# Kernel tuning notes

Hardware: AMD Instinct MI355X
Metric: run time of the kernel (lower is better)

The kernel has to match this reference:

```python
import jax, jax.numpy as jnp
import numpy as np

MEM_DIM = 256
NUM_CHILDREN = 16
BATCH = 16384


def setup_inputs() -> dict:
    key = jax.random.key(0)
    k1, k2, k3, k4, k5, k6 = jax.random.split(key, 6)
    D = MEM_DIM
    s = 1.0 / np.sqrt(D)
    return {
        "children_memory": jax.random.normal(k1, (NUM_CHILDREN, BATCH, D), jnp.float32),
        "children_hidden": jax.random.normal(k2, (NUM_CHILDREN, BATCH, D), jnp.float32),
        "Wf": jax.random.normal(k3, (D, D), jnp.float32) * s,
        "bf": jax.random.normal(k4, (D,), jnp.float32) * s,
        "Wiou": jax.random.normal(k5, (3 * D, D), jnp.float32) * s,
        "biou": jax.random.normal(k6, (3 * D,), jnp.float32) * s,
    }


def reference(children_memory, children_hidden, Wf, bf, Wiou, biou):
    D = Wf.shape[0]
    # sum of children hidden states over the child axis -> [B, D]
    hidden_sum = jnp.sum(children_hidden, axis=0)
    # per-child forget gates: [C, B, D]
    forget_gates = jax.nn.sigmoid(jnp.einsum("cbd,ed->cbe", children_hidden, Wf) + bf)
    # i/o/u gates from summed hidden: [B, 3D]
    iou = jnp.einsum("bd,ed->be", hidden_sum, Wiou) + biou
    input_gate = jax.nn.sigmoid(iou[:, :D])
    output_gate = jax.nn.sigmoid(iou[:, D:2 * D])
    memory_gate = jnp.tanh(iou[:, 2 * D:])
    node_memory = input_gate * memory_gate + jnp.sum(forget_gates * children_memory, axis=0)
    node_hidden = output_gate * jnp.tanh(node_memory)
    return node_memory, node_hidden
```

## Files before the change

kernel.cpp:

```cpp
#include <hip/hip_runtime.h>

#define CC 16
#define BB 16384
#define DD 256
#define BT 32
#define NT 512

typedef float f32x4 __attribute__((ext_vector_type(4)));
typedef short bf16x8 __attribute__((ext_vector_type(8)));

__device__ __forceinline__ unsigned short f2bf(float f) {
    unsigned u = __builtin_bit_cast(unsigned, f);
    u += 0x7fffu + ((u >> 16) & 1u);
    return (unsigned short)(u >> 16);
}

__device__ __forceinline__ bf16x8 pack8(f32x4 a, f32x4 b) {
    bf16x8 v;
    v[0] = (short)f2bf(a[0]); v[1] = (short)f2bf(a[1]);
    v[2] = (short)f2bf(a[2]); v[3] = (short)f2bf(a[3]);
    v[4] = (short)f2bf(b[0]); v[5] = (short)f2bf(b[1]);
    v[6] = (short)f2bf(b[2]); v[7] = (short)f2bf(b[3]);
    return v;
}

__device__ __forceinline__ float sigm(float x) {
    return __builtin_amdgcn_rcpf(1.0f + __expf(-x));
}
__device__ __forceinline__ float tanhf_(float x) {
    return 2.0f * __builtin_amdgcn_rcpf(1.0f + __expf(-2.0f * x)) - 1.0f;
}

__global__ __launch_bounds__(NT, 2) void treelstm(
    const float* __restrict__ cmem,
    const float* __restrict__ chid,
    const float* __restrict__ Wf,
    const float* __restrict__ bfv_g,
    const float* __restrict__ Wiou,
    const float* __restrict__ biou,
    float* __restrict__ out)
{
    __shared__ alignas(16) unsigned char Abuf[2][BT * DD * 2];

    const int tid  = threadIdx.x;
    const int lane = tid & 63;
    const int wid  = tid >> 6;
    const int l15  = lane & 15;
    const int l4   = lane >> 4;
    const int b0   = blockIdx.x * BT;
    const int wc0  = wid * 32;

    bf16x8 wfr[2][8];
#pragma unroll
    for (int n = 0; n < 2; ++n) {
        const float* wrow = Wf + (size_t)(wc0 + n * 16 + l15) * DD + l4 * 8;
#pragma unroll
        for (int k = 0; k < 8; ++k) {
            f32x4 x0 = *(const f32x4*)(wrow + k * 32);
            f32x4 x1 = *(const f32x4*)(wrow + k * 32 + 4);
            wfr[n][k] = pack8(x0, x1);
        }
    }
    float bfr[2];
#pragma unroll
    for (int n = 0; n < 2; ++n) bfr[n] = bfv_g[wc0 + n * 16 + l15];

    int sgoff[2], sloff[2];
#pragma unroll
    for (int g = 0; g < 2; ++g) {
        int gg = tid + g * NT;
        int r  = gg >> 5;
        int d0 = (gg & 31) * 8;
        sgoff[g] = (b0 + r) * DD + d0;
        sloff[g] = r * 512 + ((d0 * 2) ^ ((r & 7) << 4));
    }

    float hs[2][8];
#pragma unroll
    for (int g = 0; g < 2; ++g)
#pragma unroll
        for (int j = 0; j < 8; ++j) hs[g][j] = 0.0f;

    {
        f32x4 h0[2][2];
#pragma unroll
        for (int g = 0; g < 2; ++g) {
            const float* p = chid + sgoff[g];
            h0[g][0] = *(const f32x4*)p;
            h0[g][1] = *(const f32x4*)(p + 4);
        }
#pragma unroll
        for (int g = 0; g < 2; ++g) {
#pragma unroll
            for (int j = 0; j < 4; ++j) { hs[g][j] += h0[g][0][j]; hs[g][4 + j] += h0[g][1][j]; }
            *(bf16x8*)&Abuf[0][sloff[g]] = pack8(h0[g][0], h0[g][1]);
        }
    }
    __syncthreads();

    const int colbase = (l4 * 16) ^ ((l15 & 7) << 4);
    const int rb0 = l15 * 512;
    const int rb1 = (16 + l15) * 512;

    float nmv[2][2][4];
#pragma unroll
    for (int m = 0; m < 2; ++m)
#pragma unroll
        for (int n = 0; n < 2; ++n)
#pragma unroll
            for (int j = 0; j < 4; ++j) nmv[m][n][j] = 0.0f;

    const int cmbase = (b0 + l4 * 4) * DD + wc0 + l15;

    for (int c = 0; c < CC; ++c) {
        const float* cmc = cmem + (size_t)c * (BB * DD);
        float cmv[2][2][4];
#pragma unroll
        for (int m = 0; m < 2; ++m)
#pragma unroll
            for (int n = 0; n < 2; ++n)
#pragma unroll
                for (int j = 0; j < 4; ++j)
                    cmv[m][n][j] = cmc[cmbase + m * (16 * DD) + j * DD + n * 16];

        f32x4 hv[2][2];
        const bool more = (c + 1 < CC);
        if (more) {
            const float* hc = chid + (size_t)(c + 1) * (BB * DD);
#pragma unroll
            for (int g = 0; g < 2; ++g) {
                const float* p = hc + sgoff[g];
                hv[g][0] = *(const f32x4*)p;
                hv[g][1] = *(const f32x4*)(p + 4);
            }
        }

        f32x4 acc[2][2];
#pragma unroll
        for (int m = 0; m < 2; ++m)
#pragma unroll
            for (int n = 0; n < 2; ++n)
                acc[m][n] = (f32x4){bfr[n], bfr[n], bfr[n], bfr[n]};

        const unsigned char* bufc = &Abuf[c & 1][0];
#pragma unroll
        for (int k = 0; k < 8; ++k) {
            const int cb = colbase ^ (k << 6);
            bf16x8 a0 = *(const bf16x8*)(bufc + rb0 + cb);
            bf16x8 a1 = *(const bf16x8*)(bufc + rb1 + cb);
            acc[0][0] = __builtin_amdgcn_mfma_f32_16x16x32_bf16(a0, wfr[0][k], acc[0][0], 0, 0, 0);
            acc[0][1] = __builtin_amdgcn_mfma_f32_16x16x32_bf16(a0, wfr[1][k], acc[0][1], 0, 0, 0);
            acc[1][0] = __builtin_amdgcn_mfma_f32_16x16x32_bf16(a1, wfr[0][k], acc[1][0], 0, 0, 0);
            acc[1][1] = __builtin_amdgcn_mfma_f32_16x16x32_bf16(a1, wfr[1][k], acc[1][1], 0, 0, 0);
        }

        if (more) {
            unsigned char* bufn = &Abuf[(c & 1) ^ 1][0];
#pragma unroll
            for (int g = 0; g < 2; ++g) {
#pragma unroll
                for (int j = 0; j < 4; ++j) { hs[g][j] += hv[g][0][j]; hs[g][4 + j] += hv[g][1][j]; }
                *(bf16x8*)(bufn + sloff[g]) = pack8(hv[g][0], hv[g][1]);
            }
        }

#pragma unroll
        for (int m = 0; m < 2; ++m)
#pragma unroll
            for (int n = 0; n < 2; ++n)
#pragma unroll
                for (int j = 0; j < 4; ++j)
                    nmv[m][n][j] += sigm(acc[m][n][j]) * cmv[m][n][j];

        __syncthreads();
    }

#pragma unroll
    for (int g = 0; g < 2; ++g) {
        f32x4 a, b;
#pragma unroll
        for (int j = 0; j < 4; ++j) { a[j] = hs[g][j]; b[j] = hs[g][4 + j]; }
        *(bf16x8*)&Abuf[0][sloff[g]] = pack8(a, b);
    }
    __syncthreads();

    f32x4 gacc[3][2][2];
#pragma unroll
    for (int q = 0; q < 3; ++q) {
        bf16x8 wq[2][8];
#pragma unroll
        for (int n = 0; n < 2; ++n) {
            const float* wrow = Wiou + (size_t)(q * 256 + wc0 + n * 16 + l15) * DD + l4 * 8;
#pragma unroll
            for (int k = 0; k < 8; ++k) {
                f32x4 x0 = *(const f32x4*)(wrow + k * 32);
                f32x4 x1 = *(const f32x4*)(wrow + k * 32 + 4);
                wq[n][k] = pack8(x0, x1);
            }
        }
        float bq[2];
#pragma unroll
        for (int n = 0; n < 2; ++n) bq[n] = biou[q * 256 + wc0 + n * 16 + l15];
#pragma unroll
        for (int m = 0; m < 2; ++m)
#pragma unroll
            for (int n = 0; n < 2; ++n)
                gacc[q][m][n] = (f32x4){bq[n], bq[n], bq[n], bq[n]};

        const unsigned char* bufc = &Abuf[0][0];
#pragma unroll
        for (int k = 0; k < 8; ++k) {
            const int cb = colbase ^ (k << 6);
            bf16x8 a0 = *(const bf16x8*)(bufc + rb0 + cb);
            bf16x8 a1 = *(const bf16x8*)(bufc + rb1 + cb);
            gacc[q][0][0] = __builtin_amdgcn_mfma_f32_16x16x32_bf16(a0, wq[0][k], gacc[q][0][0], 0, 0, 0);
            gacc[q][0][1] = __builtin_amdgcn_mfma_f32_16x16x32_bf16(a0, wq[1][k], gacc[q][0][1], 0, 0, 0);
            gacc[q][1][0] = __builtin_amdgcn_mfma_f32_16x16x32_bf16(a1, wq[0][k], gacc[q][1][0], 0, 0, 0);
            gacc[q][1][1] = __builtin_amdgcn_mfma_f32_16x16x32_bf16(a1, wq[1][k], gacc[q][1][1], 0, 0, 0);
        }
    }

#pragma unroll
    for (int m = 0; m < 2; ++m)
#pragma unroll
        for (int n = 0; n < 2; ++n)
#pragma unroll
            for (int j = 0; j < 4; ++j) {
                float ig = sigm(gacc[0][m][n][j]);
                float og = sigm(gacc[1][m][n][j]);
                float ug = tanhf_(gacc[2][m][n][j]);
                float mm = nmv[m][n][j] + ig * ug;
                float hh = og * tanhf_(mm);
                int row = b0 + m * 16 + l4 * 4 + j;
                int col = wc0 + n * 16 + l15;
                out[(size_t)row * DD + col] = mm;
                out[(size_t)(BB * DD) + (size_t)row * DD + col] = hh;
            }
}

extern "C" void kernel_launch(void* const* d_in, const int* in_sizes, int n_in,
                              void* d_out, int out_size, void* d_ws, size_t ws_size,
                              hipStream_t stream) {
    const float* cmem = (const float*)d_in[0];
    const float* chid = (const float*)d_in[1];
    const float* Wf   = (const float*)d_in[2];
    const float* bf   = (const float*)d_in[3];
    const float* Wiou = (const float*)d_in[4];
    const float* biou = (const float*)d_in[5];
    float* out = (float*)d_out;

    treelstm<<<BB / BT, NT, 0, stream>>>(cmem, chid, Wf, bf, Wiou, biou, out);
}
```

Baseline: 166.8 us.

## Stream child hidden tiles straight to LDS as fp32 and halve batch tile

Child hidden rows are now copied global-to-LDS with global_load_lds in fp32, with an XOR swizzle applied on the global address, instead of being loaded into registers, converted to bf16 and stored. Conversion to bf16 moves to the LDS read side. Each wave now accumulates one slice of the hidden sum from those LDS reads. The batch tile drops from 32 to 16 rows and launch bounds rise to 4 blocks per CU to keep more loads in flight. The risk is register pressure: Wf fragments are held in registers, which can cause spills under the tighter per-thread budget. It also relies on a hand-written vmcnt wait that must match the number of outstanding loads.

```diff
diff --git a/kernel.cpp b/kernel.cpp
--- a/kernel.cpp
+++ b/kernel.cpp
@@ -3,8 +3,9 @@
 #define CC 16
 #define BB 16384
 #define DD 256
-#define BT 32
+#define BT 16
 #define NT 512
+#define SLAB ((size_t)BB * DD)
 
 typedef float f32x4 __attribute__((ext_vector_type(4)));
 typedef short bf16x8 __attribute__((ext_vector_type(8)));
@@ -31,7 +32,14 @@
     return 2.0f * __builtin_amdgcn_rcpf(1.0f + __expf(-2.0f * x)) - 1.0f;
 }
 
-__global__ __launch_bounds__(NT, 2) void treelstm(
+typedef __attribute__((address_space(3))) void lds_void;
+typedef const __attribute__((address_space(1))) void gl_void;
+
+__device__ __forceinline__ void stage16(const void* g, void* l) {
+    __builtin_amdgcn_global_load_lds((gl_void*)g, (lds_void*)l, 16, 0, 0);
+}
+
+__global__ __launch_bounds__(NT, 4) void treelstm(
     const float* __restrict__ cmem,
     const float* __restrict__ chid,
     const float* __restrict__ Wf,
@@ -40,7 +48,7 @@
     const float* __restrict__ biou,
     float* __restrict__ out)
 {
-    __shared__ alignas(16) unsigned char Abuf[2][BT * DD * 2];
+    __shared__ float hbuf[2][BT * DD];
 
     const int tid  = threadIdx.x;
     const int lane = tid & 63;
@@ -65,177 +73,137 @@
 #pragma unroll
     for (int n = 0; n < 2; ++n) bfr[n] = bfv_g[wc0 + n * 16 + l15];
 
-    int sgoff[2], sloff[2];
-#pragma unroll
-    for (int g = 0; g < 2; ++g) {
-        int gg = tid + g * NT;
-        int r  = gg >> 5;
-        int d0 = (gg & 31) * 8;
-        sgoff[g] = (b0 + r) * DD + d0;
-        sloff[g] = r * 512 + ((d0 * 2) ^ ((r & 7) << 4));
-    }
-
-    float hs[2][8];
-#pragma unroll
-    for (int g = 0; g < 2; ++g)
-#pragma unroll
-        for (int j = 0; j < 8; ++j) hs[g][j] = 0.0f;
+    const int r0 = wid * 2, r1 = r0 + 1;
+    const char* g0 = (const char*)(chid + (size_t)(b0 + r0) * DD) + ((lane * 16) ^ ((r0 & 7) << 4));
+    const char* g1 = (const char*)(chid + (size_t)(b0 + r1) * DD) + ((lane * 16) ^ ((r1 & 7) << 4));
+
+    const float* cmp = cmem + (size_t)(b0 + l4 * 4) * DD + wc0 + l15;
+
+    stage16(g0, &hbuf[0][r0 * DD]);
+    stage16(g1, &hbuf[0][r1 * DD]);
+    g0 += SLAB * 4; g1 += SLAB * 4;
+
+    float cmv[2][4];
+#pragma unroll
+    for (int n = 0; n < 2; ++n)
+#pragma unroll
+        for (int j = 0; j < 4; ++j)
+            cmv[n][j] = cmp[j * DD + n * 16];
+    const float* cmp_n = cmp + SLAB;
+
+    float hs[8];
+#pragma unroll
+    for (int j = 0; j < 8; ++j) hs[j] = 0.0f;
+    float nmv[2][4];
+#pragma unroll
+    for (int n = 0; n < 2; ++n)
+#pragma unroll
+        for (int j = 0; j < 4; ++j) nmv[n][j] = 0.0f;
+
+    const int rb = l15 * DD;
+    const int c0 = (((2 * l4) ^ (l15 & 7)) << 2);
+    const int c1 = (((2 * l4 + 1) ^ (l15 & 7)) << 2);
+
+    for (int c = 0; c < CC; ++c) {
+        asm volatile("s_waitcnt vmcnt(8)" ::: "memory");
+        __builtin_amdgcn_s_barrier();
+
+        if (c + 1 < CC) {
+            stage16(g0, &hbuf[(c + 1) & 1][r0 * DD]);
+            stage16(g1, &hbuf[(c + 1) & 1][r1 * DD]);
+            g0 += SLAB * 4; g1 += SLAB * 4;
+        }
+
+        f32x4 acc[2];
+#pragma unroll
+        for (int n = 0; n < 2; ++n)
+            acc[n] = (f32x4){bfr[n], bfr[n], bfr[n], bfr[n]};
+
+        const float* bc = &hbuf[c & 1][0];
+#pragma unroll
+        for (int kk = 0; kk < 8; ++kk) {
+            f32x4 x0 = *(const f32x4*)(bc + rb + kk * 32 + c0);
+            f32x4 x1 = *(const f32x4*)(bc + rb + kk * 32 + c1);
+            if (kk == wid) {
+#pragma unroll
+                for (int j = 0; j < 4; ++j) { hs[j] += x0[j]; hs[4 + j] += x1[j]; }
+            }
+            bf16x8 a = pack8(x0, x1);
+            acc[0] = __builtin_amdgcn_mfma_f32_16x16x32_bf16(a, wfr[0][kk], acc[0], 0, 0, 0);
+            acc[1] = __builtin_amdgcn_mfma_f32_16x16x32_bf16(a, wfr[1][kk], acc[1], 0, 0, 0);
+        }
+
+#pragma unroll
+        for (int n = 0; n < 2; ++n)
+#pragma unroll
+            for (int j = 0; j < 4; ++j)
+                nmv[n][j] += sigm(acc[n][j]) * cmv[n][j];
+
+        if (c + 1 < CC) {
+#pragma unroll
+            for (int n = 0; n < 2; ++n)
+#pragma unroll
+                for (int j = 0; j < 4; ++j)
+                    cmv[n][j] = cmp_n[j * DD + n * 16];
+            cmp_n += SLAB;
+        }
+    }
 
     {
-        f32x4 h0[2][2];
-#pragma unroll
-        for (int g = 0; g < 2; ++g) {
-            const float* p = chid + sgoff[g];
-            h0[g][0] = *(const f32x4*)p;
-            h0[g][1] = *(const f32x4*)(p + 4);
-        }
-#pragma unroll
-        for (int g = 0; g < 2; ++g) {
-#pragma unroll
-            for (int j = 0; j < 4; ++j) { hs[g][j] += h0[g][0][j]; hs[g][4 + j] += h0[g][1][j]; }
-            *(bf16x8*)&Abuf[0][sloff[g]] = pack8(h0[g][0], h0[g][1]);
-        }
+        float* hb = &hbuf[0][0];
+        f32x4 lo, hi;
+#pragma unroll
+        for (int j = 0; j < 4; ++j) { lo[j] = hs[j]; hi[j] = hs[4 + j]; }
+        *(f32x4*)(hb + rb + wid * 32 + c0) = lo;
+        *(f32x4*)(hb + rb + wid * 32 + c1) = hi;
     }
     __syncthreads();
 
-    const int colbase = (l4 * 16) ^ ((l15 & 7) << 4);
-    const int rb0 = l15 * 512;
-    const int rb1 = (16 + l15) * 512;
-
-    float nmv[2][2][4];
-#pragma unroll
-    for (int m = 0; m < 2; ++m)
-#pragma unroll
-        for (int n = 0; n < 2; ++n)
-#pragma unroll
-            for (int j = 0; j < 4; ++j) nmv[m][n][j] = 0.0f;
-
-    const int cmbase = (b0 + l4 * 4) * DD + wc0 + l15;
-
-    for (int c = 0; c < CC; ++c) {
-        const float* cmc = cmem + (size_t)c * (BB * DD);
-        float cmv[2][2][4];
-#pragma unroll
-        for (int m = 0; m < 2; ++m)
-#pragma unroll
-            for (int n = 0; n < 2; ++n)
-#pragma unroll
-                for (int j = 0; j < 4; ++j)
-                    cmv[m][n][j] = cmc[cmbase + m * (16 * DD) + j * DD + n * 16];
-
-        f32x4 hv[2][2];
-        const bool more = (c + 1 < CC);
-        if (more) {
-            const float* hc = chid + (size_t)(c + 1) * (BB * DD);
-#pragma unroll
-            for (int g = 0; g < 2; ++g) {
-                const float* p = hc + sgoff[g];
-                hv[g][0] = *(const f32x4*)p;
-                hv[g][1] = *(const f32x4*)(p + 4);
+    bf16x8 afr[8];
+    {
+        const float* hb = &hbuf[0][0];
+#pragma unroll
+        for (int kk = 0; kk < 8; ++kk) {
+            f32x4 x0 = *(const f32x4*)(hb + rb + kk * 32 + c0);
+            f32x4 x1 = *(const f32x4*)(hb + rb + kk * 32 + c1);
+            afr[kk] = pack8(x0, x1);
+        }
+    }
+
+    float gq[3][2][4];
+#pragma unroll
+    for (int q = 0; q < 3; ++q) {
+#pragma unroll
+        for (int n = 0; n < 2; ++n) {
+            const float* wrow = Wiou + (size_t)(q * DD + wc0 + n * 16 + l15) * DD + l4 * 8;
+            f32x4 acc = (f32x4){0.f, 0.f, 0.f, 0.f};
+#pragma unroll
+            for (int kk = 0; kk < 8; ++kk) {
+                f32x4 x0 = *(const f32x4*)(wrow + kk * 32);
+                f32x4 x1 = *(const f32x4*)(wrow + kk * 32 + 4);
+                bf16x8 w = pack8(x0, x1);
+                acc = __builtin_amdgcn_mfma_f32_16x16x32_bf16(afr[kk], w, acc, 0, 0, 0);
             }
-        }
-
-        f32x4 acc[2][2];
-#pragma unroll
-        for (int m = 0; m < 2; ++m)
-#pragma unroll
-            for (int n = 0; n < 2; ++n)
-                acc[m][n] = (f32x4){bfr[n], bfr[n], bfr[n], bfr[n]};
-
-        const unsigned char* bufc = &Abuf[c & 1][0];
-#pragma unroll
-        for (int k = 0; k < 8; ++k) {
-            const int cb = colbase ^ (k << 6);
-            bf16x8 a0 = *(const bf16x8*)(bufc + rb0 + cb);
-            bf16x8 a1 = *(const bf16x8*)(bufc + rb1 + cb);
-            acc[0][0] = __builtin_amdgcn_mfma_f32_16x16x32_bf16(a0, wfr[0][k], acc[0][0], 0, 0, 0);
-            acc[0][1] = __builtin_amdgcn_mfma_f32_16x16x32_bf16(a0, wfr[1][k], acc[0][1], 0, 0, 0);
-            acc[1][0] = __builtin_amdgcn_mfma_f32_16x16x32_bf16(a1, wfr[0][k], acc[1][0], 0, 0, 0);
-            acc[1][1] = __builtin_amdgcn_mfma_f32_16x16x32_bf16(a1, wfr[1][k], acc[1][1], 0, 0, 0);
-        }
-
-        if (more) {
-            unsigned char* bufn = &Abuf[(c & 1) ^ 1][0];
-#pragma unroll
-            for (int g = 0; g < 2; ++g) {
-#pragma unroll
-                for (int j = 0; j < 4; ++j) { hs[g][j] += hv[g][0][j]; hs[g][4 + j] += hv[g][1][j]; }
-                *(bf16x8*)(bufn + sloff[g]) = pack8(hv[g][0], hv[g][1]);
-            }
-        }
-
-#pragma unroll
-        for (int m = 0; m < 2; ++m)
-#pragma unroll
-            for (int n = 0; n < 2; ++n)
-#pragma unroll
-                for (int j = 0; j < 4; ++j)
-                    nmv[m][n][j] += sigm(acc[m][n][j]) * cmv[m][n][j];
-
-        __syncthreads();
-    }
-
-#pragma unroll
-    for (int g = 0; g < 2; ++g) {
-        f32x4 a, b;
-#pragma unroll
-        for (int j = 0; j < 4; ++j) { a[j] = hs[g][j]; b[j] = hs[g][4 + j]; }
-        *(bf16x8*)&Abuf[0][sloff[g]] = pack8(a, b);
-    }
-    __syncthreads();
-
-    f32x4 gacc[3][2][2];
-#pragma unroll
-    for (int q = 0; q < 3; ++q) {
-        bf16x8 wq[2][8];
-#pragma unroll
-        for (int n = 0; n < 2; ++n) {
-            const float* wrow = Wiou + (size_t)(q * 256 + wc0 + n * 16 + l15) * DD + l4 * 8;
-#pragma unroll
-            for (int k = 0; k < 8; ++k) {
-                f32x4 x0 = *(const f32x4*)(wrow + k * 32);
-                f32x4 x1 = *(const f32x4*)(wrow + k * 32 + 4);
-                wq[n][k] = pack8(x0, x1);
-            }
-        }
-        float bq[2];
-#pragma unroll
-        for (int n = 0; n < 2; ++n) bq[n] = biou[q * 256 + wc0 + n * 16 + l15];
-#pragma unroll
-        for (int m = 0; m < 2; ++m)
-#pragma unroll
-            for (int n = 0; n < 2; ++n)
-                gacc[q][m][n] = (f32x4){bq[n], bq[n], bq[n], bq[n]};
-
-        const unsigned char* bufc = &Abuf[0][0];
-#pragma unroll
-        for (int k = 0; k < 8; ++k) {
-            const int cb = colbase ^ (k << 6);
-            bf16x8 a0 = *(const bf16x8*)(bufc + rb0 + cb);
-            bf16x8 a1 = *(const bf16x8*)(bufc + rb1 + cb);
-            gacc[q][0][0] = __builtin_amdgcn_mfma_f32_16x16x32_bf16(a0, wq[0][k], gacc[q][0][0], 0, 0, 0);
-            gacc[q][0][1] = __builtin_amdgcn_mfma_f32_16x16x32_bf16(a0, wq[1][k], gacc[q][0][1], 0, 0, 0);
-            gacc[q][1][0] = __builtin_amdgcn_mfma_f32_16x16x32_bf16(a1, wq[0][k], gacc[q][1][0], 0, 0, 0);
-            gacc[q][1][1] = __builtin_amdgcn_mfma_f32_16x16x32_bf16(a1, wq[1][k], gacc[q][1][1], 0, 0, 0);
-        }
-    }
-
-#pragma unroll
-    for (int m = 0; m < 2; ++m)
-#pragma unroll
-        for (int n = 0; n < 2; ++n)
-#pragma unroll
-            for (int j = 0; j < 4; ++j) {
-                float ig = sigm(gacc[0][m][n][j]);
-                float og = sigm(gacc[1][m][n][j]);
-                float ug = tanhf_(gacc[2][m][n][j]);
-                float mm = nmv[m][n][j] + ig * ug;
-                float hh = og * tanhf_(mm);
-                int row = b0 + m * 16 + l4 * 4 + j;
-                int col = wc0 + n * 16 + l15;
-                out[(size_t)row * DD + col] = mm;
-                out[(size_t)(BB * DD) + (size_t)row * DD + col] = hh;
-            }
+            float bq = biou[q * DD + wc0 + n * 16 + l15];
+#pragma unroll
+            for (int j = 0; j < 4; ++j) gq[q][n][j] = acc[j] + bq;
+        }
+    }
+
+#pragma unroll
+    for (int n = 0; n < 2; ++n)
+#pragma unroll
+        for (int j = 0; j < 4; ++j) {
+            float ig = sigm(gq[0][n][j]);
+            float og = sigm(gq[1][n][j]);
+            float ug = tanhf_(gq[2][n][j]);
+            float mm = nmv[n][j] + ig * ug;
+            float hh = og * tanhf_(mm);
+            int row = b0 + l4 * 4 + j;
+            int col = wc0 + n * 16 + l15;
+            out[(size_t)row * DD + col] = mm;
+            out[(size_t)(BB * DD) + (size_t)row * DD + col] = hh;
+        }
 }
 
 extern "C" void kernel_launch(void* const* d_in, const int* in_sizes, int n_in,
```

Result: slower. 271.8 us (+62.9%).
